# Performance work log

Measured on AMD Instinct MI355X. Metric: run time of the kernel, lower is better.

Reference implementation:

```python
import jax, jax.numpy as jnp
import numpy as np

NEG_INF = -1e30  # stand-in for -inf that is safe under fp16/bf16 softmax


def setup_inputs() -> dict:
    key = jax.random.key(0)
    k1, k2, k3, k4 = jax.random.split(key, 4)
    B, T, C, H = 4, 4096, 1024, 64
    x = jax.random.normal(k1, (B, T, C), dtype=jnp.float32)
    Wq = jax.random.normal(k2, (C, H), dtype=jnp.float32) * (C ** -0.5)
    Wk = jax.random.normal(k3, (C, H), dtype=jnp.float32) * (C ** -0.5)
    Wv = jax.random.normal(k4, (C, H), dtype=jnp.float32) * (C ** -0.5)
    return {"x": x, "Wq": Wq, "Wk": Wk, "Wv": Wv}


def reference(x, Wq, Wk, Wv):
    # x: [B,T,C]; Wq/Wk/Wv: [C,H]
    q = jnp.einsum('btc,ch->bth', x, Wq)
    k = jnp.einsum('btc,ch->bth', x, Wk)
    v = jnp.einsum('btc,ch->bth', x, Wv)
    # NOTE: original module applies NO 1/sqrt(head_size) scaling — faithful here.
    wei = jnp.einsum('bqh,bkh->bqk', q, k)  # [B,T,T]
    T = x.shape[1]
    causal = jnp.tril(jnp.ones((T, T), dtype=bool))
    wei = jnp.where(causal, wei, NEG_INF)
    wei = jax.nn.softmax(wei, axis=-1)
    # dropout: eval-mode identity
    out = jnp.einsum('bqk,bkh->bqh', wei, v)  # [B,T,H]
    return out
```

## Files before the change

### kernel.cpp

```cpp
#include <hip/hip_runtime.h>
#include <hip/hip_fp16.h>


typedef __attribute__((ext_vector_type(8))) short bf16x8;
typedef __attribute__((ext_vector_type(8))) unsigned short u16x8;
typedef __attribute__((ext_vector_type(4))) float f32x4;

__device__ __forceinline__ unsigned short f2bf(float f) {
  unsigned u = __float_as_uint(f);
  u += 0x7fffu + ((u >> 16) & 1u);
  return (unsigned short)(u >> 16);
}
__device__ __forceinline__ float bf2f(unsigned short s) {
  return __uint_as_float(((unsigned)s) << 16);
}
__device__ __forceinline__ unsigned cvt_pk_bf16(float lo, float hi) {
  unsigned r;
  asm("v_cvt_pk_bf16_f32 %0, %1, %2" : "=v"(r) : "v"(lo), "v"(hi));
  return r;
}
__device__ __forceinline__ void gload_lds16(const void* g, void* l) {
  __builtin_amdgcn_global_load_lds(
      (const __attribute__((address_space(1))) unsigned int*)g,
      (__attribute__((address_space(3))) unsigned int*)l, 16, 0, 0);
}
#define KSWZ(row, colb) ((((row) * 128) + (colb)) ^ (((row) & 7) << 4))

__global__ __launch_bounds__(256) void wsplit_kernel(
    const float* __restrict__ Wq, const float* __restrict__ Wk,
    const float* __restrict__ Wv,
    unsigned short* __restrict__ Wth, unsigned short* __restrict__ Wtl) {
  const int fl = blockIdx.x * 256 + threadIdx.x;
  const int lane = fl & 63;
  const int rest = fl >> 6;
  const int nf = rest % 12;
  const int ksq = rest / 12;
  const int n = nf * 16 + (lane & 15);
  const int k0 = ksq * 32 + (lane >> 4) * 8;
  const float* wp = (n < 64) ? Wq : ((n < 128) ? Wk : Wv);
  const int h = n & 63;
  u16x8 hi, lo;
#pragma unroll
  for (int j = 0; j < 8; ++j) {
    float v = wp[(size_t)(k0 + j) * 64 + h];
    unsigned short hh = f2bf(v);
    hi[j] = hh;
    lo[j] = f2bf(v - bf2f(hh));
  }
  const size_t base = (size_t)fl * 8;
  *reinterpret_cast<u16x8*>(&Wth[base]) = hi;
  *reinterpret_cast<u16x8*>(&Wtl[base]) = lo;
}

__device__ __forceinline__ void cvt_store8(unsigned short* dh, unsigned short* dl,
                                           const float4& a, const float4& b) {
  float v[8] = {a.x, a.y, a.z, a.w, b.x, b.y, b.z, b.w};
  uint4 hp, lp;
  unsigned* hpp = reinterpret_cast<unsigned*>(&hp);
  unsigned* lpp = reinterpret_cast<unsigned*>(&lp);
#pragma unroll
  for (int p = 0; p < 4; ++p) {
    const unsigned h = cvt_pk_bf16(v[2 * p], v[2 * p + 1]);
    hpp[p] = h;
    const float h0 = __uint_as_float(h << 16);
    const float h1 = __uint_as_float(h & 0xffff0000u);
    lpp[p] = cvt_pk_bf16(v[2 * p] - h0, v[2 * p + 1] - h1);
  }
  *reinterpret_cast<uint4*>(dh) = hp;
  *reinterpret_cast<uint4*>(dl) = lp;
}

__global__ __launch_bounds__(256) void proj_mfma_kernel(
    const float* __restrict__ x,
    const unsigned short* __restrict__ Wth, const unsigned short* __restrict__ Wtl,
    unsigned short* __restrict__ qh, unsigned short* __restrict__ ql,
    unsigned short* __restrict__ kh, unsigned short* __restrict__ kl,
    unsigned short* __restrict__ vt) {
  __shared__ unsigned short Ah[2][64][72];
  __shared__ unsigned short Al[2][64][72];
  const int tid = threadIdx.x;
  const int w = tid >> 6;
  const int lane = tid & 63;
  const int l16 = lane & 15;
  const int g = lane >> 4;
  const int row0 = blockIdx.x * 64;
  const int sr = tid >> 2;
  const int sc = (tid & 3) * 16;

  f32x4 acc[4][3];
#pragma unroll
  for (int m = 0; m < 4; ++m)
#pragma unroll
    for (int f = 0; f < 3; ++f) {
      f32x4 z = {0.f, 0.f, 0.f, 0.f};
      acc[m][f] = z;
    }

  const float* xp = &x[(size_t)(row0 + sr) * 1024 + sc];

  float4 xs0[4], xs1[4];
#pragma unroll
  for (int i = 0; i < 4; ++i) xs0[i] = *reinterpret_cast<const float4*>(xp + i * 4);
#pragma unroll
  for (int i = 0; i < 4; ++i) xs1[i] = *reinterpret_cast<const float4*>(xp + 64 + i * 4);
  cvt_store8(&Ah[0][sr][sc], &Al[0][sr][sc], xs0[0], xs0[1]);
  cvt_store8(&Ah[0][sr][sc + 8], &Al[0][sr][sc + 8], xs0[2], xs0[3]);

  bf16x8 bhc[2][3], blc[2][3];
#pragma unroll
  for (int ks = 0; ks < 2; ++ks)
#pragma unroll
    for (int f = 0; f < 3; ++f) {
      const size_t off = ((size_t)ks * 12 + (w * 3 + f)) * 512 + lane * 8;
      bhc[ks][f] = *reinterpret_cast<const bf16x8*>(&Wth[off]);
      blc[ks][f] = *reinterpret_cast<const bf16x8*>(&Wtl[off]);
    }

#pragma unroll 2
  for (int step = 0; step < 16; ++step) {
    __syncthreads();
    bf16x8 bhn[2][3], bln[2][3];
    if (step < 15) {
#pragma unroll
      for (int ks = 0; ks < 2; ++ks)
#pragma unroll
        for (int f = 0; f < 3; ++f) {
          const size_t off =
              ((size_t)((step + 1) * 2 + ks) * 12 + (w * 3 + f)) * 512 + lane * 8;
          bhn[ks][f] = *reinterpret_cast<const bf16x8*>(&Wth[off]);
          bln[ks][f] = *reinterpret_cast<const bf16x8*>(&Wtl[off]);
        }
    }
    if (step < 14) {
      const float* px = xp + (size_t)(step + 2) * 64;
      if ((step & 1) == 0) {
#pragma unroll
        for (int i = 0; i < 4; ++i) xs0[i] = *reinterpret_cast<const float4*>(px + i * 4);
      } else {
#pragma unroll
        for (int i = 0; i < 4; ++i) xs1[i] = *reinterpret_cast<const float4*>(px + i * 4);
      }
    }
    const int cur = step & 1;
#pragma unroll
    for (int ks = 0; ks < 2; ++ks) {
      bf16x8 ah[4], al[4];
#pragma unroll
      for (int m = 0; m < 4; ++m) {
        const int ro = m * 16 + l16;
        const int co = ks * 32 + g * 8;
        ah[m] = *reinterpret_cast<const bf16x8*>(&Ah[cur][ro][co]);
        al[m] = *reinterpret_cast<const bf16x8*>(&Al[cur][ro][co]);
      }
#pragma unroll
      for (int m = 0; m < 4; ++m)
#pragma unroll
        for (int f = 0; f < 3; ++f) {
          acc[m][f] = __builtin_amdgcn_mfma_f32_16x16x32_bf16(ah[m], bhc[ks][f], acc[m][f], 0, 0, 0);
          acc[m][f] = __builtin_amdgcn_mfma_f32_16x16x32_bf16(ah[m], blc[ks][f], acc[m][f], 0, 0, 0);
          acc[m][f] = __builtin_amdgcn_mfma_f32_16x16x32_bf16(al[m], bhc[ks][f], acc[m][f], 0, 0, 0);
        }
    }
    if (step < 15) {
      if (((step + 1) & 1) == 0) {
        cvt_store8(&Ah[cur ^ 1][sr][sc], &Al[cur ^ 1][sr][sc], xs0[0], xs0[1]);
        cvt_store8(&Ah[cur ^ 1][sr][sc + 8], &Al[cur ^ 1][sr][sc + 8], xs0[2], xs0[3]);
      } else {
        cvt_store8(&Ah[cur ^ 1][sr][sc], &Al[cur ^ 1][sr][sc], xs1[0], xs1[1]);
        cvt_store8(&Ah[cur ^ 1][sr][sc + 8], &Al[cur ^ 1][sr][sc + 8], xs1[2], xs1[3]);
      }
    }
#pragma unroll
    for (int ks = 0; ks < 2; ++ks)
#pragma unroll
      for (int f = 0; f < 3; ++f) {
        bhc[ks][f] = bhn[ks][f];
        blc[ks][f] = bln[ks][f];
      }
  }

  const int b = row0 >> 12;
  const int tbase = row0 & 4095;
#pragma unroll
  for (int m = 0; m < 4; ++m)
#pragma unroll
    for (int f = 0; f < 3; ++f) {
      const int nn = w * 48 + f * 16;
      if (nn < 64) {
        const int h = nn + l16;
#pragma unroll
        for (int j = 0; j < 4; ++j) {
          const int row = row0 + m * 16 + 4 * g + j;
          const float val = acc[m][f][j];
          const unsigned short hi = f2bf(val);
          qh[(size_t)row * 64 + h] = hi;
          ql[(size_t)row * 64 + h] = f2bf(val - bf2f(hi));
        }
      } else if (nn < 128) {
        const int h = nn - 64 + l16;
#pragma unroll
        for (int j = 0; j < 4; ++j) {
          const int row = row0 + m * 16 + 4 * g + j;
          const float val = acc[m][f][j];
          const unsigned short hi = f2bf(val);
          kh[(size_t)row * 64 + h] = hi;
          kl[(size_t)row * 64 + h] = f2bf(val - bf2f(hi));
        }
      } else {
        const int h = nn - 128 + l16;
        ushort4 pv;
        pv.x = f2bf(acc[m][f][0]);
        pv.y = f2bf(acc[m][f][1]);
        pv.z = f2bf(acc[m][f][2]);
        pv.w = f2bf(acc[m][f][3]);
        const size_t a = ((size_t)b * 64 + h) * 4096 + tbase + m * 16 + 4 * g;
        *reinterpret_cast<ushort4*>(&vt[a]) = pv;
      }
    }
}

template <int PT, int NU_B>
__global__ __launch_bounds__(256) void attn_part_block_kernel(
    const unsigned short* __restrict__ qh, const unsigned short* __restrict__ ql,
    const unsigned short* __restrict__ kh, const unsigned short* __restrict__ kl,
    const unsigned short* __restrict__ vt,
    __half* __restrict__ OP, float* __restrict__ ML) {
  __shared__ __align__(16) unsigned short Khs[2][4096];
  __shared__ __align__(16) unsigned short Kls[2][4096];
  __shared__ __align__(16) unsigned short Vs[2][4096];
  __shared__ __align__(16) unsigned short pbuf[4][2][16][88];
  const int tid = threadIdx.x;
  const int w = tid >> 6;
  const int lane = tid & 63;
  const int l16 = lane & 15;
  const int g = lane >> 4;

  const int bx = blockIdx.x;
  const int xc = bx & 7;
  const int b = xc >> 1;
  const int s = 2 * (bx >> 3) + (xc & 1);
  int k = 0, pref = 0;
  for (;;) {
    const int np = (2 * k + 2 + PT - 1) / PT;
    if (s < pref + np) break;
    pref += np;
    ++k;
  }
  const int j4 = k;
  const int p = s - pref;
  const int ntiles = 2 * j4 + 2;
  const int t0 = p * PT;
  const int t1 = min(ntiles, t0 + PT);
  const int q0 = j4 * 128 + w * 32;
  const size_t rowbase = (size_t)b * 4096;

  const int te0 = w * 64 + lane;
  const int te1 = 256 + w * 64 + lane;
  const int r0_ = te0 >> 3, c80 = (te0 & 7) ^ (r0_ & 7);
  const int r1_ = te1 >> 3, c81 = (te1 & 7) ^ (r1_ & 7);
  const int lo0 = te0 * 16, lo1 = te1 * 16;

  bf16x8 q0hf[2], q0lf[2], q1hf[2], q1lf[2];
#pragma unroll
  for (int ss = 0; ss < 2; ++ss) {
    size_t a0 = (rowbase + q0 + l16) * 64 + ss * 32 + g * 8;
    q0hf[ss] = *reinterpret_cast<const bf16x8*>(&qh[a0]);
    q0lf[ss] = *reinterpret_cast<const bf16x8*>(&ql[a0]);
    size_t a1 = a0 + 16 * 64;
    q1hf[ss] = *reinterpret_cast<const bf16x8*>(&qh[a1]);
    q1lf[ss] = *reinterpret_cast<const bf16x8*>(&ql[a1]);
  }

  f32x4 o0[4], o1[4];
#pragma unroll
  for (int hb = 0; hb < 4; ++hb) {
    f32x4 z = {0.f, 0.f, 0.f, 0.f};
    o0[hb] = z;
    o1[hb] = z;
  }
  float m0 = -1e30f, l0 = 0.f, m1 = -1e30f, l1 = 0.f;

  {
    const int kv0 = t0 * 64;
    gload_lds16(&kh[(rowbase + kv0 + r0_) * 64 + c80 * 8], (char*)Khs[0] + lo0);
    gload_lds16(&kl[(rowbase + kv0 + r0_) * 64 + c80 * 8], (char*)Kls[0] + lo0);
    gload_lds16(&vt[((size_t)b * 64 + r0_) * 4096 + kv0 + c80 * 8], (char*)Vs[0] + lo0);
    gload_lds16(&kh[(rowbase + kv0 + r1_) * 64 + c81 * 8], (char*)Khs[0] + lo1);
    gload_lds16(&kl[(rowbase + kv0 + r1_) * 64 + c81 * 8], (char*)Kls[0] + lo1);
    gload_lds16(&vt[((size_t)b * 64 + r1_) * 4096 + kv0 + c81 * 8], (char*)Vs[0] + lo1);
  }

  int cur = 0;
  for (int t = t0; t < t1; ++t) {
    __syncthreads();
    if (t + 1 < t1) {
      const int kn = (t + 1) * 64;
      gload_lds16(&kh[(rowbase + kn + r0_) * 64 + c80 * 8], (char*)Khs[cur ^ 1] + lo0);
      gload_lds16(&kl[(rowbase + kn + r0_) * 64 + c80 * 8], (char*)Kls[cur ^ 1] + lo0);
      gload_lds16(&vt[((size_t)b * 64 + r0_) * 4096 + kn + c80 * 8], (char*)Vs[cur ^ 1] + lo0);
      gload_lds16(&kh[(rowbase + kn + r1_) * 64 + c81 * 8], (char*)Khs[cur ^ 1] + lo1);
      gload_lds16(&kl[(rowbase + kn + r1_) * 64 + c81 * 8], (char*)Kls[cur ^ 1] + lo1);
      gload_lds16(&vt[((size_t)b * 64 + r1_) * 4096 + kn + c81 * 8], (char*)Vs[cur ^ 1] + lo1);
    }
    const int kv0 = t * 64;

    f32x4 s0[4], s1[4];
#pragma unroll
    for (int kb = 0; kb < 4; ++kb) {
      bf16x8 khf[2], klf[2];
#pragma unroll
      for (int ss = 0; ss < 2; ++ss) {
        const int row = kb * 16 + l16;
        const int colb = ss * 64 + g * 16;
        khf[ss] = *reinterpret_cast<const bf16x8*>((const char*)Khs[cur] + KSWZ(row, colb));
        klf[ss] = *reinterpret_cast<const bf16x8*>((const char*)Kls[cur] + KSWZ(row, colb));
      }
      f32x4 a0 = {0.f, 0.f, 0.f, 0.f};
      f32x4 a1 = {0.f, 0.f, 0.f, 0.f};
#pragma unroll
      for (int ss = 0; ss < 2; ++ss) {
        a0 = __builtin_amdgcn_mfma_f32_16x16x32_bf16(khf[ss], q0hf[ss], a0, 0, 0, 0);
        a0 = __builtin_amdgcn_mfma_f32_16x16x32_bf16(khf[ss], q0lf[ss], a0, 0, 0, 0);
        a0 = __builtin_amdgcn_mfma_f32_16x16x32_bf16(klf[ss], q0hf[ss], a0, 0, 0, 0);
        a1 = __builtin_amdgcn_mfma_f32_16x16x32_bf16(khf[ss], q1hf[ss], a1, 0, 0, 0);
        a1 = __builtin_amdgcn_mfma_f32_16x16x32_bf16(khf[ss], q1lf[ss], a1, 0, 0, 0);
        a1 = __builtin_amdgcn_mfma_f32_16x16x32_bf16(klf[ss], q1hf[ss], a1, 0, 0, 0);
      }
      s0[kb] = a0;
      s1[kb] = a1;
    }
    bf16x8 vf[2][4];
#pragma unroll
    for (int ks = 0; ks < 2; ++ks)
#pragma unroll
      for (int hb = 0; hb < 4; ++hb) {
        const int row = hb * 16 + l16;
        const int colb = ks * 64 + g * 16;
        vf[ks][hb] = *reinterpret_cast<const bf16x8*>((const char*)Vs[cur] + KSWZ(row, colb));
      }
    if (kv0 + 63 > q0) {
#pragma unroll
      for (int kb = 0; kb < 4; ++kb)
#pragma unroll
        for (int jj = 0; jj < 4; ++jj) {
          const int kvg = kv0 + kb * 16 + 4 * g + jj;
          if (kvg > q0 + l16) s0[kb][jj] = -1e30f;
          if (kvg > q0 + 16 + l16) s1[kb][jj] = -1e30f;
        }
    }
    float rm0 = s0[0][0], rm1 = s1[0][0];
#pragma unroll
    for (int kb = 0; kb < 4; ++kb) {
      float c0 = fmaxf(fmaxf(s0[kb][0], s0[kb][1]), fmaxf(s0[kb][2], s0[kb][3]));
      float c1 = fmaxf(fmaxf(s1[kb][0], s1[kb][1]), fmaxf(s1[kb][2], s1[kb][3]));
      rm0 = fmaxf(rm0, c0);
      rm1 = fmaxf(rm1, c1);
    }
    rm0 = fmaxf(rm0, __shfl_xor(rm0, 16));
    rm0 = fmaxf(rm0, __shfl_xor(rm0, 32));
    rm1 = fmaxf(rm1, __shfl_xor(rm1, 16));
    rm1 = fmaxf(rm1, __shfl_xor(rm1, 32));
    const bool r0 = !__all(rm0 - m0 <= 8.f);
    const bool r1 = !__all(rm1 - m1 <= 8.f);
    const float mu0 = r0 ? fmaxf(m0, rm0) : m0;
    const float mu1 = r1 ? fmaxf(m1, rm1) : m1;
    const float al0 = r0 ? __expf(m0 - mu0) : 1.f;
    const float al1 = r1 ? __expf(m1 - mu1) : 1.f;
    float ps0 = 0.f, ps1 = 0.f;
#pragma unroll
    for (int kb = 0; kb < 4; ++kb)
#pragma unroll
      for (int jj = 0; jj < 4; ++jj) {
        const float e0 = __expf(s0[kb][jj] - mu0);
        const float e1 = __expf(s1[kb][jj] - mu1);
        s0[kb][jj] = e0;
        s1[kb][jj] = e1;
        ps0 += e0;
        ps1 += e1;
      }
    ps0 += __shfl_xor(ps0, 16);
    ps0 += __shfl_xor(ps0, 32);
    ps1 += __shfl_xor(ps1, 16);
    ps1 += __shfl_xor(ps1, 32);
    l0 = l0 * al0 + ps0;
    m0 = mu0;
    l1 = l1 * al1 + ps1;
    m1 = mu1;
#pragma unroll
    for (int kb = 0; kb < 4; ++kb) {
      *reinterpret_cast<unsigned*>(&pbuf[w][0][l16][kb * 16 + 4 * g]) =
          cvt_pk_bf16(s0[kb][0], s0[kb][1]);
      *reinterpret_cast<unsigned*>(&pbuf[w][0][l16][kb * 16 + 4 * g + 2]) =
          cvt_pk_bf16(s0[kb][2], s0[kb][3]);
      *reinterpret_cast<unsigned*>(&pbuf[w][1][l16][kb * 16 + 4 * g]) =
          cvt_pk_bf16(s1[kb][0], s1[kb][1]);
      *reinterpret_cast<unsigned*>(&pbuf[w][1][l16][kb * 16 + 4 * g + 2]) =
          cvt_pk_bf16(s1[kb][2], s1[kb][3]);
    }
    if (r0) {
#pragma unroll
      for (int jj = 0; jj < 4; ++jj) {
        const float a0r = __shfl(al0, 4 * g + jj);
#pragma unroll
        for (int hb = 0; hb < 4; ++hb) o0[hb][jj] *= a0r;
      }
    }
    if (r1) {
#pragma unroll
      for (int jj = 0; jj < 4; ++jj) {
        const float a1r = __shfl(al1, 4 * g + jj);
#pragma unroll
        for (int hb = 0; hb < 4; ++hb) o1[hb][jj] *= a1r;
      }
    }
    asm volatile("s_waitcnt lgkmcnt(0)" ::: "memory");
#pragma unroll
    for (int ks = 0; ks < 2; ++ks) {
      bf16x8 pa0 = *reinterpret_cast<const bf16x8*>(&pbuf[w][0][l16][ks * 32 + g * 8]);
      bf16x8 pa1 = *reinterpret_cast<const bf16x8*>(&pbuf[w][1][l16][ks * 32 + g * 8]);
#pragma unroll
      for (int hb = 0; hb < 4; ++hb) {
        o0[hb] = __builtin_amdgcn_mfma_f32_16x16x32_bf16(pa0, vf[ks][hb], o0[hb], 0, 0, 0);
        o1[hb] = __builtin_amdgcn_mfma_f32_16x16x32_bf16(pa1, vf[ks][hb], o1[hb], 0, 0, 0);
      }
    }
    cur ^= 1;
  }

  const size_t u = (size_t)b * NU_B + s;
  __half* op = OP + u * 8192 + (size_t)w * 32 * 64;
#pragma unroll
  for (int jj = 0; jj < 4; ++jj) {
    const int srcr = 4 * g + jj;
    const float l0r = __shfl(l0, srcr);
    const float l1r = __shfl(l1, srcr);
#pragma unroll
    for (int hb = 0; hb < 4; ++hb) {
      op[(4 * g + jj) * 64 + hb * 16 + l16] = __float2half(o0[hb][jj] / l0r);
      op[(16 + 4 * g + jj) * 64 + hb * 16 + l16] = __float2half(o1[hb][jj] / l1r);
    }
  }
  float* ml = ML + u * 256 + w * 64;
  if (lane < 16) {
    ml[lane] = m0;
    ml[32 + lane] = l0;
  } else if (lane < 32) {
    ml[lane] = m1;
    ml[32 + lane] = l1;
  }
}

template <int PT, int NU_B>
__global__ __launch_bounds__(256) void attn_combine_kernel(
    const __half* __restrict__ OP, const float* __restrict__ ML,
    float* __restrict__ out) {
  const int tid = threadIdx.x;
  const int w = tid >> 6;
  const int lane = tid & 63;
  const int rid = blockIdx.x * 4 + w;
  const int b = rid >> 12;
  const int rr = rid & 4095;
  const int j4 = rr >> 7;
  const int local = rr & 127;
  const int nparts = (2 * j4 + 2 + PT - 1) / PT;
  int prefix = 0;
  for (int k = 0; k < j4; ++k) prefix += (2 * k + 2 + PT - 1) / PT;
  const size_t base = (size_t)b * NU_B + prefix;
  const int wv = local >> 5;
  const int tile = (local >> 4) & 1;
  const int rowin = local & 15;
  const int mi = wv * 64 + tile * 16 + rowin;

  float M = -1e30f;
  for (int p = 0; p < nparts; ++p) M = fmaxf(M, ML[(base + p) * 256 + mi]);
  float wsum = 0.f, acc = 0.f;
  for (int p = 0; p < nparts; ++p) {
    const float m = ML[(base + p) * 256 + mi];
    const float l = ML[(base + p) * 256 + 32 + mi];
    const float wg = l * __expf(m - M);
    wsum += wg;
    acc += wg * __half2float(OP[(base + p) * 8192 + (size_t)local * 64 + lane]);
  }
  out[(size_t)rid * 64 + lane] = acc / wsum;
}

extern "C" void kernel_launch(void* const* d_in, const int* in_sizes, int n_in,
                              void* d_out, int out_size, void* d_ws, size_t ws_size,
                              hipStream_t stream) {
  const float* x  = (const float*)d_in[0];
  const float* Wq = (const float*)d_in[1];
  const float* Wk = (const float*)d_in[2];
  const float* Wv = (const float*)d_in[3];
  float* out = (float*)d_out;

  const size_t N = (size_t)4 * 4096 * 64;
  const size_t WN = (size_t)192 * 1024;
  unsigned short* qh = (unsigned short*)d_ws;
  unsigned short* ql = qh + N;
  unsigned short* kh = ql + N;
  unsigned short* kl = kh + N;
  unsigned short* vt = kl + N;
  unsigned short* Wth = vt + N;
  unsigned short* Wtl = Wth + WN;
  __half* OP = (__half*)(Wtl + WN);
  const size_t base_need = (5 * N + 2 * WN) * 2;

  const size_t NU4 = 4 * 272, NU8 = 4 * 144;
  const size_t need4 = base_need + NU4 * 8192 * 2 + NU4 * 256 * 4;
  const size_t need8 = base_need + NU8 * 8192 * 2 + NU8 * 256 * 4;

  wsplit_kernel<<<dim3(96), dim3(256), 0, stream>>>(Wq, Wk, Wv, Wth, Wtl);
  proj_mfma_kernel<<<dim3(256), dim3(256), 0, stream>>>(x, Wth, Wtl, qh, ql, kh, kl, vt);
  if (ws_size >= need4) {
    float* ML = (float*)(OP + NU4 * 8192);
    attn_part_block_kernel<4, 272><<<dim3(NU4), dim3(256), 0, stream>>>(qh, ql, kh, kl, vt, OP, ML);
    attn_combine_kernel<4, 272><<<dim3(4096), dim3(256), 0, stream>>>(OP, ML, out);
  } else {
    float* ML = (float*)(OP + NU8 * 8192);
    attn_part_block_kernel<8, 144><<<dim3(NU8), dim3(256), 0, stream>>>(qh, ql, kh, kl, vt, OP, ML);
    attn_combine_kernel<8, 144><<<dim3(4096), dim3(256), 0, stream>>>(OP, ML, out);
  }
}
```

Baseline: 90.87 us.

## Split projection output columns across three blocks per row tile with XCD-aware mapping

The projection kernel now launches three times as many blocks. Each block handles one third of the 192 output columns (Q, K or V portions) for a 64-row tile, so each wave computes one 16-column fragment instead of three. Block indices are remapped so the three blocks sharing a row tile land on the same XCD, letting them reuse the x tile through L2. This targets low occupancy, since 256 blocks underfill the GPU. The cost is that each block reloads and converts its x tile three times, which adds global reads and conversion work.

```diff
diff --git a/kernel.cpp b/kernel.cpp
--- a/kernel.cpp
+++ b/kernel.cpp
@@ -83,18 +83,20 @@
   const int lane = tid & 63;
   const int l16 = lane & 15;
   const int g = lane >> 4;
-  const int row0 = blockIdx.x * 64;
+  const int bx = blockIdx.x;
+  const int xcd = bx & 7;
+  const int kk = bx >> 3;
+  const int row0 = (xcd * 32 + kk / 3) * 64;
+  const int nf = (kk % 3) * 4 + w;
   const int sr = tid >> 2;
   const int sc = (tid & 3) * 16;
 
-  f32x4 acc[4][3];
-#pragma unroll
-  for (int m = 0; m < 4; ++m)
-#pragma unroll
-    for (int f = 0; f < 3; ++f) {
-      f32x4 z = {0.f, 0.f, 0.f, 0.f};
-      acc[m][f] = z;
-    }
+  f32x4 acc[4];
+#pragma unroll
+  for (int m = 0; m < 4; ++m) {
+    f32x4 z = {0.f, 0.f, 0.f, 0.f};
+    acc[m] = z;
+  }
 
   const float* xp = &x[(size_t)(row0 + sr) * 1024 + sc];
 
@@ -106,30 +108,25 @@
   cvt_store8(&Ah[0][sr][sc], &Al[0][sr][sc], xs0[0], xs0[1]);
   cvt_store8(&Ah[0][sr][sc + 8], &Al[0][sr][sc + 8], xs0[2], xs0[3]);
 
-  bf16x8 bhc[2][3], blc[2][3];
-#pragma unroll
-  for (int ks = 0; ks < 2; ++ks)
-#pragma unroll
-    for (int f = 0; f < 3; ++f) {
-      const size_t off = ((size_t)ks * 12 + (w * 3 + f)) * 512 + lane * 8;
-      bhc[ks][f] = *reinterpret_cast<const bf16x8*>(&Wth[off]);
-      blc[ks][f] = *reinterpret_cast<const bf16x8*>(&Wtl[off]);
-    }
+  bf16x8 bhc[2], blc[2];
+#pragma unroll
+  for (int ks = 0; ks < 2; ++ks) {
+    const size_t off = ((size_t)ks * 12 + nf) * 512 + lane * 8;
+    bhc[ks] = *reinterpret_cast<const bf16x8*>(&Wth[off]);
+    blc[ks] = *reinterpret_cast<const bf16x8*>(&Wtl[off]);
+  }
 
 #pragma unroll 2
   for (int step = 0; step < 16; ++step) {
     __syncthreads();
-    bf16x8 bhn[2][3], bln[2][3];
+    bf16x8 bhn[2], bln[2];
     if (step < 15) {
 #pragma unroll
-      for (int ks = 0; ks < 2; ++ks)
-#pragma unroll
-        for (int f = 0; f < 3; ++f) {
-          const size_t off =
-              ((size_t)((step + 1) * 2 + ks) * 12 + (w * 3 + f)) * 512 + lane * 8;
-          bhn[ks][f] = *reinterpret_cast<const bf16x8*>(&Wth[off]);
-          bln[ks][f] = *reinterpret_cast<const bf16x8*>(&Wtl[off]);
-        }
+      for (int ks = 0; ks < 2; ++ks) {
+        const size_t off = ((size_t)((step + 1) * 2 + ks) * 12 + nf) * 512 + lane * 8;
+        bhn[ks] = *reinterpret_cast<const bf16x8*>(&Wth[off]);
+        bln[ks] = *reinterpret_cast<const bf16x8*>(&Wtl[off]);
+      }
     }
     if (step < 14) {
       const float* px = xp + (size_t)(step + 2) * 64;
@@ -153,13 +150,11 @@
         al[m] = *reinterpret_cast<const bf16x8*>(&Al[cur][ro][co]);
       }
 #pragma unroll
-      for (int m = 0; m < 4; ++m)
-#pragma unroll
-        for (int f = 0; f < 3; ++f) {
-          acc[m][f] = __builtin_amdgcn_mfma_f32_16x16x32_bf16(ah[m], bhc[ks][f], acc[m][f], 0, 0, 0);
-          acc[m][f] = __builtin_amdgcn_mfma_f32_16x16x32_bf16(ah[m], blc[ks][f], acc[m][f], 0, 0, 0);
-          acc[m][f] = __builtin_amdgcn_mfma_f32_16x16x32_bf16(al[m], bhc[ks][f], acc[m][f], 0, 0, 0);
-        }
+      for (int m = 0; m < 4; ++m) {
+        acc[m] = __builtin_amdgcn_mfma_f32_16x16x32_bf16(ah[m], bhc[ks], acc[m], 0, 0, 0);
+        acc[m] = __builtin_amdgcn_mfma_f32_16x16x32_bf16(ah[m], blc[ks], acc[m], 0, 0, 0);
+        acc[m] = __builtin_amdgcn_mfma_f32_16x16x32_bf16(al[m], bhc[ks], acc[m], 0, 0, 0);
+      }
     }
     if (step < 15) {
       if (((step + 1) & 1) == 0) {
@@ -171,52 +166,52 @@
       }
     }
 #pragma unroll
-    for (int ks = 0; ks < 2; ++ks)
-#pragma unroll
-      for (int f = 0; f < 3; ++f) {
-        bhc[ks][f] = bhn[ks][f];
-        blc[ks][f] = bln[ks][f];
-      }
+    for (int ks = 0; ks < 2; ++ks) {
+      bhc[ks] = bhn[ks];
+      blc[ks] = bln[ks];
+    }
   }
 
   const int b = row0 >> 12;
   const int tbase = row0 & 4095;
-#pragma unroll
-  for (int m = 0; m < 4; ++m)
-#pragma unroll
-    for (int f = 0; f < 3; ++f) {
-      const int nn = w * 48 + f * 16;
-      if (nn < 64) {
-        const int h = nn + l16;
-#pragma unroll
-        for (int j = 0; j < 4; ++j) {
-          const int row = row0 + m * 16 + 4 * g + j;
-          const float val = acc[m][f][j];
-          const unsigned short hi = f2bf(val);
-          qh[(size_t)row * 64 + h] = hi;
-          ql[(size_t)row * 64 + h] = f2bf(val - bf2f(hi));
-        }
-      } else if (nn < 128) {
-        const int h = nn - 64 + l16;
-#pragma unroll
-        for (int j = 0; j < 4; ++j) {
-          const int row = row0 + m * 16 + 4 * g + j;
-          const float val = acc[m][f][j];
-          const unsigned short hi = f2bf(val);
-          kh[(size_t)row * 64 + h] = hi;
-          kl[(size_t)row * 64 + h] = f2bf(val - bf2f(hi));
-        }
-      } else {
-        const int h = nn - 128 + l16;
-        ushort4 pv;
-        pv.x = f2bf(acc[m][f][0]);
-        pv.y = f2bf(acc[m][f][1]);
-        pv.z = f2bf(acc[m][f][2]);
-        pv.w = f2bf(acc[m][f][3]);
-        const size_t a = ((size_t)b * 64 + h) * 4096 + tbase + m * 16 + 4 * g;
-        *reinterpret_cast<ushort4*>(&vt[a]) = pv;
-      }
-    }
+  const int nn = nf * 16;
+  if (nn < 64) {
+    const int h = nn + l16;
+#pragma unroll
+    for (int m = 0; m < 4; ++m)
+#pragma unroll
+      for (int j = 0; j < 4; ++j) {
+        const int row = row0 + m * 16 + 4 * g + j;
+        const float val = acc[m][j];
+        const unsigned short hi = f2bf(val);
+        qh[(size_t)row * 64 + h] = hi;
+        ql[(size_t)row * 64 + h] = f2bf(val - bf2f(hi));
+      }
+  } else if (nn < 128) {
+    const int h = nn - 64 + l16;
+#pragma unroll
+    for (int m = 0; m < 4; ++m)
+#pragma unroll
+      for (int j = 0; j < 4; ++j) {
+        const int row = row0 + m * 16 + 4 * g + j;
+        const float val = acc[m][j];
+        const unsigned short hi = f2bf(val);
+        kh[(size_t)row * 64 + h] = hi;
+        kl[(size_t)row * 64 + h] = f2bf(val - bf2f(hi));
+      }
+  } else {
+    const int h = nn - 128 + l16;
+#pragma unroll
+    for (int m = 0; m < 4; ++m) {
+      ushort4 pv;
+      pv.x = f2bf(acc[m][0]);
+      pv.y = f2bf(acc[m][1]);
+      pv.z = f2bf(acc[m][2]);
+      pv.w = f2bf(acc[m][3]);
+      const size_t a = ((size_t)b * 64 + h) * 4096 + tbase + m * 16 + 4 * g;
+      *reinterpret_cast<ushort4*>(&vt[a]) = pv;
+    }
+  }
 }
 
 template <int PT, int NU_B>
@@ -510,7 +505,7 @@
   const size_t need8 = base_need + NU8 * 8192 * 2 + NU8 * 256 * 4;
 
   wsplit_kernel<<<dim3(96), dim3(256), 0, stream>>>(Wq, Wk, Wv, Wth, Wtl);
-  proj_mfma_kernel<<<dim3(256), dim3(256), 0, stream>>>(x, Wth, Wtl, qh, ql, kh, kl, vt);
+  proj_mfma_kernel<<<dim3(768), dim3(256), 0, stream>>>(x, Wth, Wtl, qh, ql, kh, kl, vt);
   if (ws_size >= need4) {
     float* ML = (float*)(OP + NU4 * 8192);
     attn_part_block_kernel<4, 272><<<dim3(NU4), dim3(256), 0, stream>>>(qh, ql, kh, kl, vt, OP, ML);
```

Result: slower. 93.72 us (+3.1%).
